# Optimization experiments

Hardware: AMD Instinct MI355X
Metric: run time of the kernel (lower is better)

The kernel has to match this reference:

```python
import jax, jax.numpy as jnp
import numpy as np

INPUT_DIM = 1024
LATENT_DIM = 16 * INPUT_DIM
K_VALUES = (32, 128, 256)


def setup_inputs() -> dict:
    key = jax.random.key(0)
    ks = jax.random.split(key, 7)
    B = 4096
    x = jax.random.normal(ks[0], (B, INPUT_DIM), dtype=jnp.float32)
    MLP_output = jax.random.normal(ks[1], (B, INPUT_DIM), dtype=jnp.float32)
    # encoder: nn.Linear(input_dim, latent_dim) -> weight [latent, input], bias zeroed in __init__
    W_enc = jax.random.normal(ks[2], (LATENT_DIM, INPUT_DIM), dtype=jnp.float32) / np.sqrt(INPUT_DIM)
    b_enc = jnp.zeros((LATENT_DIM,), dtype=jnp.float32)
    # decoder / skip / b_dec are zeros in __init__, but use small random values so the
    # reference exercises non-trivial math (zeros would make decode degenerate)
    W_dec = jax.random.normal(ks[3], (LATENT_DIM, INPUT_DIM), dtype=jnp.float32) * 0.02
    b_dec = jax.random.normal(ks[4], (INPUT_DIM,), dtype=jnp.float32) * 0.02
    W_skip = jax.random.normal(ks[5], (INPUT_DIM, INPUT_DIM), dtype=jnp.float32) * 0.02
    return {"x": x, "MLP_output": MLP_output, "W_enc": W_enc, "b_enc": b_enc,
            "W_dec": W_dec, "b_dec": b_dec, "W_skip": W_skip}


def _topk_relu(z, k):
    # keep top-k per row, relu the kept values, zero elsewhere (scatter)
    vals, idx = jax.lax.top_k(z, k)                     # [B, k]
    vals = jax.nn.relu(vals)
    rows = jnp.arange(z.shape[0])[:, None]              # [B, 1]
    return jnp.zeros_like(z).at[rows, idx].set(vals)


def reference(x, MLP_output, W_enc, b_enc, W_dec, b_dec, W_skip):
    B = x.shape[0]
    pre = x @ W_enc.T + b_enc                            # [B, latent] (shared across k)
    skip = x @ W_skip + b_dec                            # [B, input]
    total_variance = jnp.sum((x - x.mean(0)) ** 2)

    mean_encoded = jnp.zeros((B, LATENT_DIM), dtype=x.dtype)
    mean_decoded = jnp.zeros((B, INPUT_DIM), dtype=x.dtype)
    total_loss = jnp.asarray(0.0, dtype=x.dtype)
    encoded = None
    for k in K_VALUES:                                   # fixed small set of k values
        encoded = _topk_relu(pre, k)                     # [B, latent]
        decoded = encoded @ W_dec + skip                 # [B, input]
        mean_encoded = mean_encoded + encoded
        mean_decoded = mean_decoded + decoded
        total_loss = total_loss + jnp.sum((MLP_output - decoded) ** 2)

    n = float(len(K_VALUES))
    mean_encoded = mean_encoded / n
    mean_decoded = mean_decoded / n
    total_loss = total_loss / total_variance
    # l0 over the last (k=256) encoded tensor
    l0_norm_final = jnp.sum(jnp.count_nonzero(encoded, axis=0))
    return (mean_encoded, mean_decoded, total_loss, l0_norm_final)
```

## Files before the change

kernel.cpp:

```cpp
#include <hip/hip_runtime.h>
#include <stdint.h>

typedef short   bf16x8 __attribute__((ext_vector_type(8)));
typedef float   f32x4  __attribute__((ext_vector_type(4)));
typedef float   f32x16 __attribute__((ext_vector_type(16)));
typedef int     i32x4  __attribute__((ext_vector_type(4)));
typedef int     i32x8  __attribute__((ext_vector_type(8)));
typedef unsigned short u16x8 __attribute__((ext_vector_type(8)));
typedef unsigned long long u64;
typedef long long i64;
typedef long long i64x2 __attribute__((ext_vector_type(2)));

#define B_ROWS 4096
#define D_IN   1024
#define L_DIM  16384
#define NBIN   2048
#define CCAP   1024
#define SLOTS  32
#define W8SCALE 1200.0f

__device__ __forceinline__ unsigned short f2bf(float f) {
  unsigned int u = __float_as_uint(f);
  u = (u + 0x7FFFu + ((u >> 16) & 1u)) >> 16;
  return (unsigned short)u;
}
__device__ __forceinline__ float bf2f(unsigned short h) {
  return __uint_as_float(((unsigned int)h) << 16);
}
__device__ __forceinline__ unsigned char f2e4m3(float v) {
  unsigned int u = __float_as_uint(v);
  unsigned int s = (u >> 24) & 0x80u;
  unsigned int a = u & 0x7FFFFFFFu;
  unsigned int r = (a + 0x0007FFFFu + ((a >> 20) & 1u)) >> 20;
  if (r <= (120u << 3)) return (unsigned char)s;
  r -= (120u << 3);
  if (r > 0x7Eu) r = 0x7Eu;
  return (unsigned char)(s | r);
}
__device__ __forceinline__ float e4m3f(unsigned char b) {
  unsigned int e = (b >> 3) & 0xFu, m = b & 7u, s = ((unsigned int)b & 0x80u) << 24;
  if (e == 0) return __uint_as_float(s);
  return __uint_as_float(s | ((e + 120u) << 23) | (m << 20));
}
__device__ __forceinline__ unsigned int sortkey(float f) {
  unsigned int u = __float_as_uint(f);
  return (u & 0x80000000u) ? ~u : (u | 0x80000000u);
}
__device__ __forceinline__ float keyval(unsigned int k) {
  unsigned int u = (k & 0x80000000u) ? (k & 0x7FFFFFFFu) : ~k;
  return __uint_as_float(u);
}
__device__ __forceinline__ int binof(float v) {
  int b = (int)((v + 2.0f) * (2048.0f / 7.0f));
  return b < 0 ? 0 : (b > 2047 ? 2047 : b);
}
__device__ __forceinline__ void gl_lds16(const void* g, void* l) {
  __builtin_amdgcn_global_load_lds(
      (const __attribute__((address_space(1))) unsigned int*)g,
      (__attribute__((address_space(3))) unsigned int*)l, 16, 0, 0);
}
__device__ __forceinline__ float waveSum(float v) {
  #pragma unroll
  for (int m = 32; m; m >>= 1) v += __shfl_xor(v, m);
  return v;
}

__global__ void k_zero(float* scal, float* colsum, float* colsq, unsigned int* rowcnt) {
  int t = blockIdx.x * blockDim.x + threadIdx.x;
  if (t < 8) scal[t] = 0.f;
  if (t < 1024) { colsum[t] = 0.f; colsq[t] = 0.f; }
  for (int i = t; i < B_ROWS; i += gridDim.x * blockDim.x) rowcnt[i] = 0u;
}

__global__ void k_convert(const float* __restrict__ in, unsigned short* __restrict__ out, int n4) {
  int i = blockIdx.x * blockDim.x + threadIdx.x;
  int stride = gridDim.x * blockDim.x;
  for (; i < n4; i += stride) {
    f32x4 v = *((const f32x4*)in + i);
    ushort4 o;
    o.x = f2bf(v[0]); o.y = f2bf(v[1]); o.z = f2bf(v[2]); o.w = f2bf(v[3]);
    *((ushort4*)out + i) = o;
  }
}

__global__ void k_convert_fp8(const float* __restrict__ in, unsigned char* __restrict__ out, int n4) {
  int i = blockIdx.x * blockDim.x + threadIdx.x;
  int stride = gridDim.x * blockDim.x;
  for (; i < n4; i += stride) {
    f32x4 v = *((const f32x4*)in + i);
    unsigned int u = 0;
    #pragma unroll
    for (int j = 0; j < 4; j++) u |= ((unsigned int)f2e4m3(v[j])) << (8 * j);
    *((unsigned int*)out + i) = u;
  }
}

__global__ void k_convert_i8(const float* __restrict__ in, unsigned int* __restrict__ out, int n4) {
  int i = blockIdx.x * blockDim.x + threadIdx.x;
  int stride = gridDim.x * blockDim.x;
  for (; i < n4; i += stride) {
    f32x4 v = *((const f32x4*)in + i);
    unsigned int u = 0;
    #pragma unroll
    for (int j = 0; j < 4; j++) {
      int q = (int)rintf(v[j] * W8SCALE);
      q = q > 127 ? 127 : (q < -127 ? -127 : q);
      u |= ((unsigned int)q & 0xFFu) << (8 * j);
    }
    out[i] = u;
  }
}

__global__ void k_transpose_bf(const float* __restrict__ in, unsigned short* __restrict__ out, int n) {
  __shared__ float tile[32][33];
  int bx = blockIdx.x * 32, by = blockIdx.y * 32;
  int tx = threadIdx.x, ty = threadIdx.y;
  tile[ty][tx] = in[(size_t)(by + ty) * n + bx + tx];
  __syncthreads();
  out[(size_t)(bx + ty) * n + by + tx] = f2bf(tile[tx][ty]);
}

__global__ __launch_bounds__(256) void k_var1(const float* __restrict__ x, float* colsum, float* colsq) {
  int g = blockIdx.x;
  int t = threadIdx.x;
  float s[4] = {0,0,0,0}, q[4] = {0,0,0,0};
  for (int r = 0; r < 32; r++) {
    const float* rp = x + (size_t)(g * 32 + r) * D_IN;
    #pragma unroll
    for (int j = 0; j < 4; j++) {
      float v = rp[t + 256 * j];
      s[j] += v; q[j] += v * v;
    }
  }
  #pragma unroll
  for (int j = 0; j < 4; j++) {
    atomicAdd(&colsum[t + 256 * j], s[j]);
    atomicAdd(&colsq [t + 256 * j], q[j]);
  }
}

__global__ __launch_bounds__(256) void k_var2(const float* colsum, const float* colsq, float* scal) {
  __shared__ float red[4];
  int t = threadIdx.x;
  float loc = 0.f;
  #pragma unroll
  for (int j = 0; j < 4; j++) {
    int c = t + 256 * j;
    float cs = colsum[c], cq = colsq[c];
    loc += cq - cs * cs * (1.f / (float)B_ROWS);
  }
  loc = waveSum(loc);
  if ((t & 63) == 0) red[t >> 6] = loc;
  __syncthreads();
  if (t == 0) scal[1] = red[0] + red[1] + red[2] + red[3];
}

__device__ __forceinline__ void stage_half8(const unsigned char* __restrict__ G,
                                            int Kb, int r0, int k0b,
                                            unsigned char* buf, int t) {
  #pragma unroll
  for (int j = 0; j < 2; j++) {
    int q = j * 256 + t;
    int row = q >> 2, u = q & 3;
    int uu = u ^ ((row >> 1) & 3);
    gl_lds16(&G[(size_t)(r0 + row) * Kb + k0b + uu * 16], &buf[q * 16]);
  }
}

__global__ __launch_bounds__(256, 3) void k_gemm_enc(
    const unsigned char* __restrict__ A8, const unsigned char* __restrict__ B8,
    const float* __restrict__ bias,
    u64* __restrict__ cand, unsigned int* __restrict__ rowcnt,
    int M, int N, int K) {
  __shared__ unsigned char sBuf[3 * 16384];
  unsigned int*  stageKey = (unsigned int*)sBuf;
  unsigned char* stageCol = (unsigned char*)&sBuf[16384];
  unsigned int*  s_cnt    = (unsigned int*)&sBuf[20480];
  unsigned int*  s_base   = (unsigned int*)&sBuf[21504];

  const int t = threadIdx.x;
  const int w = t >> 6, l = t & 63;
  const int wr = w >> 1, wc = w & 1;
  const int lr = l & 31, lh = l >> 5;
  const int row0 = blockIdx.y * 128, col0 = blockIdx.x * 128;
  const int Kb = K;
  const int NT = K >> 6;

  f32x16 acc[2][2] = {};

  stage_half8(A8, Kb, row0, 0,   sBuf + 0,             t);
  stage_half8(B8, Kb, col0, 0,   sBuf + 8192,          t);
  stage_half8(A8, Kb, row0, 64,  sBuf + 16384,         t);
  stage_half8(B8, Kb, col0, 64,  sBuf + 16384 + 8192,  t);

  const int raf = wr * 64 + lr,  swa = (raf >> 1) & 3;
  const int rbf = wc * 64 + lr,  swb = (rbf >> 1) & 3;
  const int uA0 = ((2 * lh)     ^ swa) * 16, uA1 = ((2 * lh + 1) ^ swa) * 16;
  const int uB0 = ((2 * lh)     ^ swb) * 16, uB1 = ((2 * lh + 1) ^ swb) * 16;
  const int offA0 = raf * 64,        offA1 = (raf + 32) * 64;
  const int offB0 = 8192 + rbf * 64, offB1 = 8192 + (rbf + 32) * 64;

  for (int tt = 0; tt < NT; tt++) {
    asm volatile("s_waitcnt vmcnt(4)" ::: "memory");
    __builtin_amdgcn_s_barrier();

    int ks = (tt + 2 < NT) ? (tt + 2) : (NT - 1);
    unsigned char* nb = sBuf + ((tt + 2) % 3) * 16384;
    stage_half8(A8, Kb, row0, ks * 64, nb, t);
    stage_half8(B8, Kb, col0, ks * 64, nb + 8192, t);

    const unsigned char* cb = sBuf + (tt % 3) * 16384;

    union Frag { i32x8 w; i32x4 h[2]; };
    Frag av[2], bv[2];
    av[0].h[0] = *(const i32x4*)&cb[offA0 + uA0];
    av[0].h[1] = *(const i32x4*)&cb[offA0 + uA1];
    av[1].h[0] = *(const i32x4*)&cb[offA1 + uA0];
    av[1].h[1] = *(const i32x4*)&cb[offA1 + uA1];
    bv[0].h[0] = *(const i32x4*)&cb[offB0 + uB0];
    bv[0].h[1] = *(const i32x4*)&cb[offB0 + uB1];
    bv[1].h[0] = *(const i32x4*)&cb[offB1 + uB0];
    bv[1].h[1] = *(const i32x4*)&cb[offB1 + uB1];

    __builtin_amdgcn_s_setprio(1);
    #pragma unroll
    for (int mt = 0; mt < 2; mt++)
      #pragma unroll
      for (int nt = 0; nt < 2; nt++)
        acc[mt][nt] = __builtin_amdgcn_mfma_scale_f32_32x32x64_f8f6f4(
            av[mt].w, bv[nt].w, acc[mt][nt],
            0, 0,
            0, 0x7F7F7F7Fu,
            0, 0x7F7F7F7Fu);
    __builtin_amdgcn_s_setprio(0);
  }

  asm volatile("s_waitcnt vmcnt(0) lgkmcnt(0)" ::: "memory");
  __syncthreads();

  if (t < 128) s_cnt[t] = 0u;
  __syncthreads();

  #pragma unroll
  for (int nt = 0; nt < 2; nt++) {
    int cl = wc * 64 + nt * 32 + lr;
    float bvs = bias[col0 + cl];
    #pragma unroll
    for (int mt = 0; mt < 2; mt++) {
      int rbase = wr * 64 + mt * 32 + lh * 4;
      #pragma unroll
      for (int i = 0; i < 16; i++) {
        float v = acc[mt][nt][i] + bvs;
        if (v > 1.7f) {
          int r = rbase + (i & 3) + 8 * (i >> 2);
          unsigned int p = atomicAdd(&s_cnt[r], 1u);
          if (p < SLOTS) {
            stageKey[r * SLOTS + p] = sortkey(v);
            stageCol[r * SLOTS + p] = (unsigned char)cl;
          }
        }
      }
    }
  }
  __syncthreads();

  if (t < 128) {
    unsigned int c = s_cnt[t];
    if (c > SLOTS)      { atomicAdd(&rowcnt[row0 + t], 4096u); s_base[t] = 0x80000000u; }
    else if (c)         s_base[t] = atomicAdd(&rowcnt[row0 + t], c);
    else                s_base[t] = 0u;
  }
  __syncthreads();

  for (int s = t; s < 128 * SLOTS; s += 256) {
    int r = s >> 5, p = s & (SLOTS - 1);
    unsigned int c = s_cnt[r], g0 = s_base[r];
    if ((unsigned int)p < c && c <= SLOTS && !(g0 & 0x80000000u)) {
      unsigned int g = g0 + (unsigned int)p;
      if (g < CCAP)
        cand[(size_t)(row0 + r) * CCAP + g] =
            ((u64)stageKey[s] << 32) | (unsigned int)(~(unsigned int)(col0 + stageCol[s]));
    }
  }
}

__device__ __forceinline__ void stage_swz(const unsigned short* __restrict__ G, int ld,
                                          int r0, int k0, unsigned short* lds, int t) {
  #pragma unroll
  for (int j = 0; j < 4; j++) {
    int q = j * 256 + t;
    int row = q >> 3, u = q & 7;
    int uu = u ^ (row & 7);
    gl_lds16(&G[(size_t)(r0 + row) * ld + k0 + uu * 8], &lds[q * 8]);
  }
}

__device__ __forceinline__ void gemm_core(
    const unsigned short* __restrict__ A, const unsigned short* __restrict__ Bm,
    unsigned short* sA, unsigned short* sB,
    int row0, int col0, int K, int t, int wr, int wc, int lm, int u0,
    f32x4 acc[4][4]) {
  for (int k0 = 0; k0 < K; k0 += 64) {
    stage_swz(A,  K, row0, k0, sA, t);
    stage_swz(Bm, K, col0, k0, sB, t);
    __syncthreads();
    bf16x8 af[4][2], bfr[4][2];
    #pragma unroll
    for (int i = 0; i < 4; i++) {
      int r = wr * 64 + i * 16 + lm;
      int sw = r & 7;
      af[i][0] = *(const bf16x8*)&sA[r * 64 + ((u0 ^ sw) * 8)];
      af[i][1] = *(const bf16x8*)&sA[r * 64 + (((u0 + 4) ^ sw) * 8)];
    }
    #pragma unroll
    for (int n = 0; n < 4; n++) {
      int r = wc * 64 + n * 16 + lm;
      int sw = r & 7;
      bfr[n][0] = *(const bf16x8*)&sB[r * 64 + ((u0 ^ sw) * 8)];
      bfr[n][1] = *(const bf16x8*)&sB[r * 64 + (((u0 + 4) ^ sw) * 8)];
    }
    #pragma unroll
    for (int i = 0; i < 4; i++)
      #pragma unroll
      for (int n = 0; n < 4; n++) {
        acc[i][n] = __builtin_amdgcn_mfma_f32_16x16x32_bf16(af[i][0], bfr[n][0], acc[i][n], 0, 0, 0);
        acc[i][n] = __builtin_amdgcn_mfma_f32_16x16x32_bf16(af[i][1], bfr[n][1], acc[i][n], 0, 0, 0);
      }
    __syncthreads();
  }
}

__global__ __launch_bounds__(256) void k_gemm_skip(
    const unsigned short* __restrict__ A, const unsigned short* __restrict__ Bm,
    const float* __restrict__ bias, unsigned short* __restrict__ Cb,
    int M, int N, int K) {
  __shared__ unsigned short sA[128 * 64];
  __shared__ unsigned short sB[128 * 64];
  const int t = threadIdx.x;
  const int w = t >> 6, l = t & 63;
  const int wr = w >> 1, wc = w & 1;
  const int lm = l & 15, u0 = l >> 4;
  const int row0 = blockIdx.y * 128, col0 = blockIdx.x * 128;

  f32x4 acc[4][4] = {};
  gemm_core(A, Bm, sA, sB, row0, col0, K, t, wr, wc, lm, u0, acc);

  const int lg = l >> 4;
  #pragma unroll
  for (int n = 0; n < 4; n++) {
    int col = col0 + wc * 64 + n * 16 + lm;
    float bv = bias[col];
    #pragma unroll
    for (int i = 0; i < 4; i++) {
      int rbase = row0 + wr * 64 + i * 16 + lg * 4;
      #pragma unroll
      for (int j = 0; j < 4; j++)
        Cb[(size_t)(rbase + j) * N + col] = f2bf(acc[i][n][j] + bv);
    }
  }
}

__global__ __launch_bounds__(256) void k_select(
    const u64* __restrict__ cand, const unsigned int* __restrict__ rowcnt,
    const unsigned char* __restrict__ xf8, const unsigned char* __restrict__ wenc8,
    const float* __restrict__ benc,
    float* __restrict__ menc, uint2* __restrict__ lists, unsigned int* __restrict__ l0p) {
  __shared__ u64 sc[CCAP];
  __shared__ unsigned int hist[NBIN];
  __shared__ u64 scratch[256];
  __shared__ unsigned int sS[256];
  __shared__ uint2 win[256];
  __shared__ int s_bb[3];
  __shared__ unsigned int s_bc[3];
  __shared__ u64 s_T[3];
  __shared__ int s_scnt;
  __shared__ unsigned int s_l0, s_pos;

  const int b = blockIdx.x, t = threadIdx.x;
  float* rowp = menc + (size_t)b * L_DIM;

  int cnt = (int)rowcnt[b];
  if (cnt >= 256 && cnt <= CCAP) {
    for (int i = t; i < cnt; i += 256) sc[i] = cand[(size_t)b * CCAP + i];
    #pragma unroll 4
    for (int g = 0; g < 16; g++) {
      f32x4 z = {};
      *(f32x4*)&rowp[g * 1024 + t * 4] = z;
    }
    __syncthreads();
  } else {
    unsigned char* xrow = (unsigned char*)scratch;
    for (int i = t; i < D_IN; i += 256) xrow[i] = xf8[(size_t)b * D_IN + i];
    __syncthreads();
    for (int q = 0; q < 64; q++) {
      int lat = q * 256 + t;
      const unsigned char* wp = &wenc8[(size_t)lat * D_IN];
      float a = 0.f;
      for (int k = 0; k < D_IN; k++) a += e4m3f(xrow[k]) * e4m3f(wp[k]);
      rowp[lat] = a + benc[lat];
    }
    __syncthreads();
    float T = 1.7f;
    for (int at = 0; at < 10; at++) {
      if (t == 0) s_scnt = 0;
      __syncthreads();
      int loc = 0;
      for (int q = 0; q < 64; q++) loc += (rowp[q * 256 + t] > T) ? 1 : 0;
      atomicAdd(&s_scnt, loc);
      __syncthreads();
      int c2 = s_scnt;
      if (c2 >= 256 && c2 <= CCAP) break;
      T = (c2 < 256) ? (T - 0.5f) : (T + 0.3f);
      __syncthreads();
    }
    if (t == 0) s_scnt = 0;
    __syncthreads();
    for (int q = 0; q < 64; q++) {
      int lat = q * 256 + t;
      float v = rowp[lat];
      if (v > T) {
        int p = atomicAdd(&s_scnt, 1);
        if (p < CCAP) sc[p] = ((u64)sortkey(v) << 32) | (unsigned int)(~(unsigned int)lat);
      }
    }
    __syncthreads();
    cnt = min(s_scnt, CCAP);
    for (int i = t * 4; i < L_DIM; i += 1024) { f32x4 z = {}; *(f32x4*)&rowp[i] = z; }
    __syncthreads();
  }

  for (int i = t; i < NBIN; i += 256) hist[i] = 0u;
  __syncthreads();
  for (int i = t; i < cnt; i += 256) {
    float v = keyval((unsigned int)(sc[i] >> 32));
    atomicAdd(&hist[binof(v)], 1u);
  }
  __syncthreads();

  unsigned int csum = 0;
  #pragma unroll
  for (int j = 0; j < 8; j++) csum += hist[t * 8 + j];
  sS[t] = csum;
  __syncthreads();
  for (int off = 1; off < 256; off <<= 1) {
    unsigned int v2 = (t + off < 256) ? sS[t + off] : 0u;
    __syncthreads();
    sS[t] += v2;
    __syncthreads();
  }
  {
    unsigned int above = (t < 255) ? sS[t + 1] : 0u;
    unsigned int run = 0;
    for (int j = 7; j >= 0; j--) {
      int bb = t * 8 + j;
      unsigned int S = above + run, h = hist[bb];
      if (h) {
        if (S < 32u  && 32u  <= S + h) { s_bb[0] = bb; s_bc[0] = S; }
        if (S < 128u && 128u <= S + h) { s_bb[1] = bb; s_bc[1] = S; }
        if (S < 256u && 256u <= S + h) { s_bb[2] = bb; s_bc[2] = S; }
      }
      run += h;
    }
  }
  __syncthreads();

  for (int ri = 0; ri < 3; ri++) {
    const int r = (ri == 0) ? 32 : (ri == 1) ? 128 : 256;
    int bb = s_bb[ri];
    int cA = (int)s_bc[ri];
    if (t == 0) s_scnt = 0;
    __syncthreads();
    for (int i = t; i < cnt; i += 256) {
      float v = keyval((unsigned int)(sc[i] >> 32));
      if (binof(v) == bb) {
        int p = atomicAdd(&s_scnt, 1);
        if (p < 256) scratch[p] = sc[i];
      }
    }
    __syncthreads();
    int m = min(s_scnt, 256);
    for (int i = t; i < m; i += 256) {
      u64 me = scratch[i];
      int rk = 0;
      for (int j2 = 0; j2 < m; j2++) rk += (scratch[j2] > me) ? 1 : 0;
      if (rk == r - cA - 1) s_T[ri] = me;
    }
    __syncthreads();
  }

  if (t == 0) { s_pos = 0u; s_l0 = 0u; }
  __syncthreads();
  const u64 T32 = s_T[0], T128 = s_T[1], T256 = s_T[2];
  for (int i = t; i < cnt; i += 256) {
    u64 e = sc[i];
    int w = (e >= T32) ? 3 : (e >= T128) ? 2 : (e >= T256) ? 1 : 0;
    if (w) {
      unsigned int p = atomicAdd(&s_pos, 1u);
      int idx = (int)(~(unsigned int)e) & (L_DIM - 1);
      float v = keyval((unsigned int)(e >> 32));
      float rv = fmaxf(v, 0.f);
      if (p < 256u)
        win[p] = make_uint2((unsigned int)idx | ((unsigned int)w << 20), __float_as_uint(rv));
      if (rv > 0.f) atomicAdd(&s_l0, 1u);
    }
  }
  __syncthreads();
  for (int i = (int)s_pos + t; i < 256; i += 256) win[i] = make_uint2(0xFFFFFu, 0u);
  __syncthreads();

  for (int k = 2; k <= 256; k <<= 1) {
    for (int j = k >> 1; j > 0; j >>= 1) {
      int x = t ^ j;
      if (x > t) {
        uint2 a = win[t], bb2 = win[x];
        bool asc = ((t & k) == 0);
        bool swap = asc ? ((a.x & 0xFFFFFu) > (bb2.x & 0xFFFFFu))
                        : ((a.x & 0xFFFFFu) < (bb2.x & 0xFFFFFu));
        if (swap) { win[t] = bb2; win[x] = a; }
      }
      __syncthreads();
    }
  }

  lists[(size_t)b * 256 + t] = win[t];

  {
    uint2 e = win[t];
    int idx = (int)(e.x & 0xFFFFFu) & (L_DIM - 1);
    unsigned int wg = (e.x >> 20) & 3u;
    float rv = __uint_as_float(e.y);
    rowp[idx] = rv * (float)wg * (1.f / 3.f);
  }

  if (t == 0) atomicAdd(l0p, s_l0);
}

__global__ __launch_bounds__(512) void k_decode(
    const uint2* __restrict__ lists, const unsigned char* __restrict__ W8,
    const unsigned short* __restrict__ skipb, const float* __restrict__ mlp,
    float* __restrict__ mdec, float* __restrict__ loss_acc) {
  __shared__ uint2 ll[256];
  __shared__ float part[3][128][25];
  __shared__ float red[2];
  const int b = blockIdx.x, t = threadIdx.x;
  if (t < 256) ll[t] = lists[(size_t)b * 256 + t];
  __syncthreads();

  const int lane = t & 127, grp = t >> 7;
  const int c = lane * 8;

  float a1[8] = {}, a2[8] = {}, a3[8] = {};

  #pragma unroll 4
  for (int i = 0; i < 64; i++) {
    uint2 e = ll[4 * i + grp];
    int idx = (int)(e.x & 0xFFFFFu) & (L_DIM - 1);
    int wgt = (int)((e.x >> 20) & 3u);
    float v = __uint_as_float(e.y) * (1.0f / W8SCALE);
    uint2 qw = *(const uint2*)&W8[(size_t)idx * D_IN + c];
    float f[8];
    #pragma unroll
    for (int j = 0; j < 4; j++) {
      f[j]     = (float)((int)(qw.x << (24 - 8 * j)) >> 24);
      f[4 + j] = (float)((int)(qw.y << (24 - 8 * j)) >> 24);
    }
    if (wgt == 3) {
      #pragma unroll
      for (int j = 0; j < 8; j++) a1[j] += v * f[j];
    } else if (wgt == 2) {
      #pragma unroll
      for (int j = 0; j < 8; j++) a2[j] += v * f[j];
    } else {
      #pragma unroll
      for (int j = 0; j < 8; j++) a3[j] += v * f[j];
    }
  }

  if (grp != 0) {
    #pragma unroll
    for (int j = 0; j < 8; j++) {
      part[grp - 1][lane][j]      = a1[j];
      part[grp - 1][lane][8 + j]  = a2[j];
      part[grp - 1][lane][16 + j] = a3[j];
    }
  }
  __syncthreads();

  float lsum = 0.f;
  if (grp == 0) {
    #pragma unroll
    for (int g = 0; g < 3; g++) {
      #pragma unroll
      for (int j = 0; j < 8; j++) {
        a1[j] += part[g][lane][j];
        a2[j] += part[g][lane][8 + j];
        a3[j] += part[g][lane][16 + j];
      }
    }
    u16x8 skv = *(const u16x8*)&skipb[(size_t)b * D_IN + c];
    f32x4 m0 = *(const f32x4*)&mlp[(size_t)b * D_IN + c];
    f32x4 m1 = *(const f32x4*)&mlp[(size_t)b * D_IN + c + 4];
    float mm[8] = {m0[0], m0[1], m0[2], m0[3], m1[0], m1[1], m1[2], m1[3]};
    float md[8];
    #pragma unroll
    for (int j = 0; j < 8; j++) {
      float sk   = bf2f(skv[j]);
      float d32  = sk + a1[j];
      float d128 = d32 + a2[j];
      float d256 = d128 + a3[j];
      md[j] = (d32 + d128 + d256) * (1.f / 3.f);
      float e1 = mm[j] - d32, e2 = mm[j] - d128, e3 = mm[j] - d256;
      lsum += e1 * e1 + e2 * e2 + e3 * e3;
    }
    f32x4 o0 = {md[0], md[1], md[2], md[3]};
    f32x4 o1 = {md[4], md[5], md[6], md[7]};
    *(f32x4*)&mdec[(size_t)b * D_IN + c]     = o0;
    *(f32x4*)&mdec[(size_t)b * D_IN + c + 4] = o1;
  }

  lsum = waveSum(lsum);
  if ((t & 63) == 0 && t < 128) red[t >> 6] = lsum;
  __syncthreads();
  if (t == 0) atomicAdd(loss_acc, red[0] + red[1]);
}

__global__ void k_final(const float* scal, const unsigned int* l0p, float* outscal) {
  outscal[0] = scal[0] / scal[1];
  outscal[1] = (float)(*l0p);
}

extern "C" void kernel_launch(void* const* d_in, const int* in_sizes, int n_in,
                              void* d_out, int out_size, void* d_ws, size_t ws_size,
                              hipStream_t stream) {
  (void)in_sizes; (void)n_in; (void)out_size; (void)ws_size;
  const float* x     = (const float*)d_in[0];
  const float* mlp   = (const float*)d_in[1];
  const float* Wenc  = (const float*)d_in[2];
  const float* benc  = (const float*)d_in[3];
  const float* Wdec  = (const float*)d_in[4];
  const float* bdec  = (const float*)d_in[5];
  const float* Wskip = (const float*)d_in[6];

  char* ws = (char*)d_ws;
  float*          scal    = (float*)(ws + 0);
  unsigned int*   l0p     = (unsigned int*)(ws + 8);
  float*          colsum  = (float*)(ws + 256);
  float*          colsq   = (float*)(ws + 4352);
  unsigned int*   rowcnt  = (unsigned int*)(ws + 8448);
  unsigned short* xb      = (unsigned short*)(ws + 24832);
  unsigned char*  wenc8   = (unsigned char*)(ws + 8413440);
  unsigned char*  xf8     = (unsigned char*)(ws + 8413440 + 16777216);
  unsigned short* wsktb   = (unsigned short*)(ws + 41967872);
  unsigned short* skipb   = (unsigned short*)(ws + 44065024);
  uint2*          lists   = (uint2*)(ws + 52453632);
  u64*            cand    = (u64*)(ws + 60842240);
  unsigned char*  wdec8   = (unsigned char*)(ws + 60842240);

  float* out  = (float*)d_out;
  float* menc = out;
  float* mdec = out + (size_t)B_ROWS * L_DIM;
  float* oscl = out + (size_t)B_ROWS * L_DIM + (size_t)B_ROWS * D_IN;

  k_zero<<<16, 256, 0, stream>>>(scal, colsum, colsq, rowcnt);
  k_convert<<<2048, 256, 0, stream>>>(x, xb, (B_ROWS * D_IN) / 4);
  k_convert_fp8<<<1024, 256, 0, stream>>>(x,    xf8,   (B_ROWS * D_IN) / 4);
  k_convert_fp8<<<2048, 256, 0, stream>>>(Wenc, wenc8, (L_DIM * D_IN) / 4);
  k_transpose_bf<<<dim3(32, 32), dim3(32, 32), 0, stream>>>(Wskip, wsktb, D_IN);
  k_var1<<<128, 256, 0, stream>>>(x, colsum, colsq);
  k_var2<<<1, 256, 0, stream>>>(colsum, colsq, scal);
  k_gemm_enc<<<dim3(L_DIM / 128, B_ROWS / 128), 256, 0, stream>>>(
      xf8, wenc8, benc, cand, rowcnt, B_ROWS, L_DIM, D_IN);
  k_gemm_skip<<<dim3(D_IN / 128, B_ROWS / 128), 256, 0, stream>>>(
      xb, wsktb, bdec, skipb, B_ROWS, D_IN, D_IN);
  k_select<<<B_ROWS, 256, 0, stream>>>(cand, rowcnt, xf8, wenc8, benc, menc, lists, l0p);
  k_convert_i8<<<2048, 256, 0, stream>>>(Wdec, (unsigned int*)wdec8, (L_DIM * D_IN) / 4);
  k_decode<<<B_ROWS, 512, 0, stream>>>(lists, wdec8, skipb, mlp, mdec, scal);
  k_final<<<1, 1, 0, stream>>>(scal, l0p, oscl);
}
```

Before: 488.8 us.

## Fuse x conversions with variance pass; prefetch and offset-encode int8 decoder weights

Merges the bf16 and fp8 conversions of x with the column sum and sum-of-squares pass into one kernel, so x is read once instead of three times and two launches go away. The decoder weights are now stored as unsigned int8 with a +128 offset. The decode loop converts them with plain zero-extending byte extracts and packed float2 FMAs, then removes the offset at the end by subtracting 128 times the sum of the values in each group. The decode loop also prefetches the next entry's weight row using readfirstlane on the index, and the partial-sum LDS row gets one more word of padding so 8-byte accesses stay aligned. The offset correction adds float cancellation error, and the readfirstlane assumes each wave reads a uniform list entry.

```diff
diff --git a/kernel.cpp b/kernel.cpp
--- a/kernel.cpp
+++ b/kernel.cpp
@@ -2,6 +2,7 @@
 #include <stdint.h>
 
 typedef short   bf16x8 __attribute__((ext_vector_type(8)));
+typedef float   f32x2  __attribute__((ext_vector_type(2)));
 typedef float   f32x4  __attribute__((ext_vector_type(4)));
 typedef float   f32x16 __attribute__((ext_vector_type(16)));
 typedef int     i32x4  __attribute__((ext_vector_type(4)));
@@ -72,14 +73,30 @@
   for (int i = t; i < B_ROWS; i += gridDim.x * blockDim.x) rowcnt[i] = 0u;
 }
 
-__global__ void k_convert(const float* __restrict__ in, unsigned short* __restrict__ out, int n4) {
-  int i = blockIdx.x * blockDim.x + threadIdx.x;
-  int stride = gridDim.x * blockDim.x;
-  for (; i < n4; i += stride) {
-    f32x4 v = *((const f32x4*)in + i);
-    ushort4 o;
-    o.x = f2bf(v[0]); o.y = f2bf(v[1]); o.z = f2bf(v[2]); o.w = f2bf(v[3]);
-    *((ushort4*)out + i) = o;
+__global__ __launch_bounds__(256) void k_prep_x(const float* __restrict__ x,
+    unsigned short* __restrict__ xb, unsigned char* __restrict__ xf8,
+    float* colsum, float* colsq) {
+  const int g = blockIdx.x;
+  const int t = threadIdx.x;
+  const int c0 = t * 4;
+  float s[4] = {0,0,0,0}, q[4] = {0,0,0,0};
+  for (int r = 0; r < 16; r++) {
+    size_t row = (size_t)g * 16 + r;
+    f32x4 v = *(const f32x4*)&x[row * D_IN + c0];
+    ushort4 ob;
+    ob.x = f2bf(v[0]); ob.y = f2bf(v[1]); ob.z = f2bf(v[2]); ob.w = f2bf(v[3]);
+    *(ushort4*)&xb[row * D_IN + c0] = ob;
+    unsigned int u = 0;
+    #pragma unroll
+    for (int j = 0; j < 4; j++) u |= ((unsigned int)f2e4m3(v[j])) << (8 * j);
+    *(unsigned int*)&xf8[row * D_IN + c0] = u;
+    #pragma unroll
+    for (int j = 0; j < 4; j++) { s[j] += v[j]; q[j] += v[j] * v[j]; }
+  }
+  #pragma unroll
+  for (int j = 0; j < 4; j++) {
+    atomicAdd(&colsum[c0 + j], s[j]);
+    atomicAdd(&colsq [c0 + j], q[j]);
   }
 }
 
@@ -105,7 +122,7 @@
     for (int j = 0; j < 4; j++) {
       int q = (int)rintf(v[j] * W8SCALE);
       q = q > 127 ? 127 : (q < -127 ? -127 : q);
-      u |= ((unsigned int)q & 0xFFu) << (8 * j);
+      u |= (((unsigned int)(q + 128)) & 0xFFu) << (8 * j);
     }
     out[i] = u;
   }
@@ -118,25 +135,6 @@
   tile[ty][tx] = in[(size_t)(by + ty) * n + bx + tx];
   __syncthreads();
   out[(size_t)(bx + ty) * n + by + tx] = f2bf(tile[tx][ty]);
-}
-
-__global__ __launch_bounds__(256) void k_var1(const float* __restrict__ x, float* colsum, float* colsq) {
-  int g = blockIdx.x;
-  int t = threadIdx.x;
-  float s[4] = {0,0,0,0}, q[4] = {0,0,0,0};
-  for (int r = 0; r < 32; r++) {
-    const float* rp = x + (size_t)(g * 32 + r) * D_IN;
-    #pragma unroll
-    for (int j = 0; j < 4; j++) {
-      float v = rp[t + 256 * j];
-      s[j] += v; q[j] += v * v;
-    }
-  }
-  #pragma unroll
-  for (int j = 0; j < 4; j++) {
-    atomicAdd(&colsum[t + 256 * j], s[j]);
-    atomicAdd(&colsq [t + 256 * j], q[j]);
-  }
 }
 
 __global__ __launch_bounds__(256) void k_var2(const float* colsum, const float* colsq, float* scal) {
@@ -540,7 +538,7 @@
     const unsigned short* __restrict__ skipb, const float* __restrict__ mlp,
     float* __restrict__ mdec, float* __restrict__ loss_acc) {
   __shared__ uint2 ll[256];
-  __shared__ float part[3][128][25];
+  __shared__ float part[3][128][26];
   __shared__ float red[2];
   const int b = blockIdx.x, t = threadIdx.x;
   if (t < 256) ll[t] = lists[(size_t)b * 256 + t];
@@ -549,39 +547,60 @@
   const int lane = t & 127, grp = t >> 7;
   const int c = lane * 8;
 
-  float a1[8] = {}, a2[8] = {}, a3[8] = {};
+  f32x2 a1[4] = {}, a2[4] = {}, a3[4] = {};
+  float vs3 = 0.f, vs2 = 0.f, vs1 = 0.f;
+
+  uint2 e = ll[grp];
+  uint2 qw = *(const uint2*)&W8[
+      ((size_t)(__builtin_amdgcn_readfirstlane(e.x) & (L_DIM - 1))) * D_IN + c];
 
   #pragma unroll 4
   for (int i = 0; i < 64; i++) {
-    uint2 e = ll[4 * i + grp];
-    int idx = (int)(e.x & 0xFFFFFu) & (L_DIM - 1);
-    int wgt = (int)((e.x >> 20) & 3u);
+    unsigned int ex = __builtin_amdgcn_readfirstlane(e.x);
+    int wgt = (int)((ex >> 20) & 3u);
     float v = __uint_as_float(e.y) * (1.0f / W8SCALE);
-    uint2 qw = *(const uint2*)&W8[(size_t)idx * D_IN + c];
-    float f[8];
+
+    uint2 e_n = ll[4 * ((i + 1) & 63) + grp];
+    uint2 qw_n = *(const uint2*)&W8[
+        ((size_t)(__builtin_amdgcn_readfirstlane(e_n.x) & (L_DIM - 1))) * D_IN + c];
+
+    f32x2 f[4];
+    f[0][0] = (float)(qw.x & 0xFFu);          f[0][1] = (float)((qw.x >> 8) & 0xFFu);
+    f[1][0] = (float)((qw.x >> 16) & 0xFFu);  f[1][1] = (float)(qw.x >> 24);
+    f[2][0] = (float)(qw.y & 0xFFu);          f[2][1] = (float)((qw.y >> 8) & 0xFFu);
+    f[3][0] = (float)((qw.y >> 16) & 0xFFu);  f[3][1] = (float)(qw.y >> 24);
+    f32x2 vv; vv[0] = v; vv[1] = v;
+
+    if (wgt == 3) {
+      vs3 += v;
+      #pragma unroll
+      for (int j = 0; j < 4; j++) a1[j] += vv * f[j];
+    } else if (wgt == 2) {
+      vs2 += v;
+      #pragma unroll
+      for (int j = 0; j < 4; j++) a2[j] += vv * f[j];
+    } else {
+      vs1 += v;
+      #pragma unroll
+      for (int j = 0; j < 4; j++) a3[j] += vv * f[j];
+    }
+    e = e_n; qw = qw_n;
+  }
+
+  {
+    f32x2 c1; c1[0] = 128.f * vs3; c1[1] = c1[0];
+    f32x2 c2; c2[0] = 128.f * vs2; c2[1] = c2[0];
+    f32x2 c3; c3[0] = 128.f * vs1; c3[1] = c3[0];
+    #pragma unroll
+    for (int j = 0; j < 4; j++) { a1[j] -= c1; a2[j] -= c2; a3[j] -= c3; }
+  }
+
+  if (grp != 0) {
     #pragma unroll
     for (int j = 0; j < 4; j++) {
-      f[j]     = (float)((int)(qw.x << (24 - 8 * j)) >> 24);
-      f[4 + j] = (float)((int)(qw.y << (24 - 8 * j)) >> 24);
-    }
-    if (wgt == 3) {
-      #pragma unroll
-      for (int j = 0; j < 8; j++) a1[j] += v * f[j];
-    } else if (wgt == 2) {
-      #pragma unroll
-      for (int j = 0; j < 8; j++) a2[j] += v * f[j];
-    } else {
-      #pragma unroll
-      for (int j = 0; j < 8; j++) a3[j] += v * f[j];
-    }
-  }
-
-  if (grp != 0) {
-    #pragma unroll
-    for (int j = 0; j < 8; j++) {
-      part[grp - 1][lane][j]      = a1[j];
-      part[grp - 1][lane][8 + j]  = a2[j];
-      part[grp - 1][lane][16 + j] = a3[j];
+      *(f32x2*)&part[grp - 1][lane][2 * j]      = a1[j];
+      *(f32x2*)&part[grp - 1][lane][8 + 2 * j]  = a2[j];
+      *(f32x2*)&part[grp - 1][lane][16 + 2 * j] = a3[j];
     }
   }
   __syncthreads();
@@ -591,10 +610,10 @@
     #pragma unroll
     for (int g = 0; g < 3; g++) {
       #pragma unroll
-      for (int j = 0; j < 8; j++) {
-        a1[j] += part[g][lane][j];
-        a2[j] += part[g][lane][8 + j];
-        a3[j] += part[g][lane][16 + j];
+      for (int j = 0; j < 4; j++) {
+        a1[j] += *(const f32x2*)&part[g][lane][2 * j];
+        a2[j] += *(const f32x2*)&part[g][lane][8 + 2 * j];
+        a3[j] += *(const f32x2*)&part[g][lane][16 + 2 * j];
       }
     }
     u16x8 skv = *(const u16x8*)&skipb[(size_t)b * D_IN + c];
@@ -604,10 +623,11 @@
     float md[8];
     #pragma unroll
     for (int j = 0; j < 8; j++) {
+      float A1 = a1[j >> 1][j & 1], A2 = a2[j >> 1][j & 1], A3 = a3[j >> 1][j & 1];
       float sk   = bf2f(skv[j]);
-      float d32  = sk + a1[j];
-      float d128 = d32 + a2[j];
-      float d256 = d128 + a3[j];
+      float d32  = sk + A1;
+      float d128 = d32 + A2;
+      float d256 = d128 + A3;
       md[j] = (d32 + d128 + d256) * (1.f / 3.f);
       float e1 = mm[j] - d32, e2 = mm[j] - d128, e3 = mm[j] - d256;
       lsum += e1 * e1 + e2 * e2 + e3 * e3;
@@ -662,11 +682,9 @@
   float* oscl = out + (size_t)B_ROWS * L_DIM + (size_t)B_ROWS * D_IN;
 
   k_zero<<<16, 256, 0, stream>>>(scal, colsum, colsq, rowcnt);
-  k_convert<<<2048, 256, 0, stream>>>(x, xb, (B_ROWS * D_IN) / 4);
-  k_convert_fp8<<<1024, 256, 0, stream>>>(x,    xf8,   (B_ROWS * D_IN) / 4);
+  k_prep_x<<<256, 256, 0, stream>>>(x, xb, xf8, colsum, colsq);
   k_convert_fp8<<<2048, 256, 0, stream>>>(Wenc, wenc8, (L_DIM * D_IN) / 4);
   k_transpose_bf<<<dim3(32, 32), dim3(32, 32), 0, stream>>>(Wskip, wsktb, D_IN);
-  k_var1<<<128, 256, 0, stream>>>(x, colsum, colsq);
   k_var2<<<1, 256, 0, stream>>>(colsum, colsq, scal);
   k_gemm_enc<<<dim3(L_DIM / 128, B_ROWS / 128), 256, 0, stream>>>(
       xf8, wenc8, benc, cand, rowcnt, B_ROWS, L_DIM, D_IN);
```

New measurement: 508.7 us. 4.1% more time.
